# Kernel tuning notes

Measured on AMD Instinct MI355X. Metric: run time of the kernel, lower is better.

The kernel has to match this reference:

```python
import jax, jax.numpy as jnp
import numpy as np

N = 10000      # nodes
E = 320000     # edges (avg degree 32)
G = 32         # graphs in batch
L = 6          # layers
C0, C1, C2 = 128, 64, 32   # irreps channels: 128x0e + 64x1e + 32x2e
H = 4          # attention heads
NB = 128       # radial basis
RAD = 64       # radial MLP width (fc_neurons=[64,64])
F = 512        # irreps_feature = 512x0e
T = 1          # num_targets
MAXR = 5.0


def setup_inputs() -> dict:
    key = jax.random.key(0)
    ks = iter(jax.random.split(key, 64))
    def nrm(shape, scale):
        return jax.random.normal(next(ks), shape, jnp.float32) * scale
    inp = {}
    inp['pos'] = jax.random.normal(next(ks), (N, 3), jnp.float32) * 3.0
    inp['node_atom'] = jax.random.randint(next(ks), (N,), 0, 5)
    inp['batch'] = jnp.sort(jax.random.randint(next(ks), (N,), 0, G))
    inp['edge_src'] = jax.random.randint(next(ks), (E,), 0, N)
    inp['edge_dst'] = jax.random.randint(next(ks), (E,), 0, N)
    inp['atom_emb'] = nrm((5, C0), 1.0)
    inp['Wrad1'] = nrm((L, NB, RAD), NB ** -0.5)
    inp['brad1'] = jnp.zeros((L, RAD), jnp.float32)
    inp['Wrad2'] = nrm((L, RAD, RAD), RAD ** -0.5)
    inp['brad2'] = jnp.zeros((L, RAD), jnp.float32)
    inp['Ws_src'] = nrm((L, C0, C0), C0 ** -0.5)
    inp['Ww_s'] = nrm((L, RAD, C0), RAD ** -0.5)
    inp['Ws_v'] = nrm((L, C0, C1), C0 ** -0.5)
    inp['Ww_v'] = nrm((L, RAD, C1), RAD ** -0.5)
    inp['Wv_v'] = nrm((L, C1, C1), C1 ** -0.5)
    inp['Ww_vv'] = nrm((L, RAD, C1), RAD ** -0.5)
    inp['Ws_t'] = nrm((L, C0, C2), C0 ** -0.5)
    inp['Ww_t'] = nrm((L, RAD, C2), RAD ** -0.5)
    inp['Wt_t'] = nrm((L, C2, C2), C2 ** -0.5)
    inp['Ww_tt'] = nrm((L, RAD, C2), RAD ** -0.5)
    inp['attn_a'] = nrm((L, H, C0 // H), (C0 // H) ** -0.5)
    inp['Wo_s'] = nrm((L, C0, C0), C0 ** -0.5)
    inp['Wo_v'] = nrm((L, C1, C1), C1 ** -0.5)
    inp['Wo_t'] = nrm((L, C2, C2), C2 ** -0.5)
    inp['g_s'] = jnp.ones((L, C0), jnp.float32)
    inp['b_s'] = jnp.zeros((L, C0), jnp.float32)
    inp['g_v'] = jnp.ones((L, C1), jnp.float32)
    inp['g_t'] = jnp.ones((L, C2), jnp.float32)
    inp['W_feat'] = nrm((C0, F), C0 ** -0.5)
    inp['b_feat'] = jnp.zeros((F,), jnp.float32)
    inp['W_out1'] = nrm((F, 1), F ** -0.5)
    inp['b_out1'] = jnp.zeros((1,), jnp.float32)
    inp['W_read'] = nrm((1, T), 1.0)
    inp['b_read'] = jnp.zeros((T,), jnp.float32)
    return inp


def reference(pos, node_atom, batch, edge_src, edge_dst, atom_emb,
              Wrad1, brad1, Wrad2, brad2, Ws_src, Ww_s, Ws_v, Ww_v,
              Wv_v, Ww_vv, Ws_t, Ww_t, Wt_t, Ww_tt, attn_a,
              Wo_s, Wo_v, Wo_t, g_s, b_s, g_v, g_t,
              W_feat, b_feat, W_out1, b_out1, W_read, b_read):
    eps = 1e-6
    # node features per irrep: scalars s [N,C0], vectors v [N,C1,3], l=2 t [N,C2,5]
    s = atom_emb[node_atom]
    v = jnp.zeros((N, C1, 3), s.dtype)
    t = jnp.zeros((N, C2, 5), s.dtype)
    # edge geometry (shared across layers)
    rel = pos[edge_dst] - pos[edge_src]            # [E,3]
    d = jnp.sqrt(jnp.sum(rel * rel, -1) + eps)     # [E]
    u = rel / d[:, None]
    centers = jnp.linspace(0.0, MAXR, NB)
    width = MAXR / NB
    rbf = jnp.exp(-0.5 * ((d[:, None] - centers[None, :]) / width) ** 2)  # [E,NB]
    x_, y_, z_ = u[:, 0], u[:, 1], u[:, 2]
    s3, s5, s15 = jnp.sqrt(3.0), jnp.sqrt(5.0), jnp.sqrt(15.0)
    sh1 = s3 * u                                   # [E,3]  l=1 spherical harmonics
    sh2 = jnp.stack([s15 * x_ * y_, s15 * y_ * z_, 0.5 * s5 * (3 * z_ * z_ - 1.0),
                     s15 * x_ * z_, 0.5 * s15 * (x_ * x_ - y_ * y_)], -1)  # [E,5]
    for l in range(L):
        # radial MLP on RBF -> per-edge tensor-product weights
        w = jax.nn.silu(jax.nn.silu(rbf @ Wrad1[l] + brad1[l]) @ Wrad2[l] + brad2[l])  # [E,RAD]
        s_e = s[edge_src]
        # tensor-product messages: 0e x Yl paths + self (l x 0e) paths
        msg_s = (s_e @ Ws_src[l]) * (w @ Ww_s[l])                                        # [E,C0]
        msg_v = ((s_e @ Ws_v[l]) * (w @ Ww_v[l]))[:, :, None] * sh1[:, None, :] \
              + jnp.einsum('eci,cd->edi', v[edge_src], Wv_v[l]) * (w @ Ww_vv[l])[:, :, None]  # [E,C1,3]
        msg_t = ((s_e @ Ws_t[l]) * (w @ Ww_t[l]))[:, :, None] * sh2[:, None, :] \
              + jnp.einsum('ecm,cd->edm', t[edge_src], Wt_t[l]) * (w @ Ww_tt[l])[:, :, None]  # [E,C2,5]
        # multi-head attention over incoming edges (softmax per dst node)
        msg_sh = msg_s.reshape(E, H, C0 // H)
        logit = jnp.einsum('ehc,hc->eh', msg_sh, attn_a[l])                              # [E,H]
        mx = jax.ops.segment_max(logit, edge_dst, num_segments=N)
        ex = jnp.exp(logit - mx[edge_dst])
        den = jax.ops.segment_sum(ex, edge_dst, num_segments=N) + 1e-9
        alpha = ex / den[edge_dst]                                                       # [E,H]
        agg_s = jax.ops.segment_sum(alpha[:, :, None] * msg_sh, edge_dst, num_segments=N).reshape(N, C0)
        agg_v = jax.ops.segment_sum(alpha[:, :, None, None] * msg_v.reshape(E, H, C1 // H, 3),
                                    edge_dst, num_segments=N).reshape(N, C1, 3)
        agg_t = jax.ops.segment_sum(alpha[:, :, None, None] * msg_t.reshape(E, H, C2 // H, 5),
                                    edge_dst, num_segments=N).reshape(N, C2, 5)
        # output projection + residual
        s = s + agg_s @ Wo_s[l]
        v = v + jnp.einsum('nci,cd->ndi', agg_v, Wo_v[l])
        t = t + jnp.einsum('ncm,cd->ndm', agg_t, Wo_t[l])
        # equivariant layer norm
        mu = jnp.mean(s, -1, keepdims=True)
        var = jnp.mean((s - mu) ** 2, -1, keepdims=True)
        s = (s - mu) / jnp.sqrt(var + eps) * g_s[l] + b_s[l]
        v = v / jnp.sqrt(jnp.mean(jnp.sum(v * v, -1), -1) + eps)[:, None, None] * g_v[l][None, :, None]
        t = t / jnp.sqrt(jnp.mean(jnp.sum(t * t, -1), -1) + eps)[:, None, None] * g_t[l][None, :, None]
    # 512x0e feature head -> per-node scalar -> sum pool per graph -> readout Linear(1,T)
    feat = jax.nn.gelu(s @ W_feat + b_feat)
    node_e = feat @ W_out1 + b_out1                      # [N,1]
    graph = jax.ops.segment_sum(node_e, batch, num_segments=G)  # [G,1]
    return graph @ W_read + b_read                       # [G,T]
```

## Files before the change

### kernel.cpp

```cpp
#include <hip/hip_runtime.h>
#include <math.h>

#define NN 10000
#define EE 320000
#define GG 32
#define LL 6
#define TABN 2048
#define TABB (TABN / 64)
#define DTAB 5.45f
#define DCUT 5.4f

__device__ __forceinline__ float fsilu(float x) { return x / (1.0f + __expf(-x)); }
__device__ __forceinline__ float fgelu(float x) {
  float y = 0.7978845608f * (x + 0.044715f * x * x * x);
  float t = 1.0f - 2.0f / (__expf(2.0f * y) + 1.0f);
  return 0.5f * x * (1.0f + t);
}

__global__ void k_hist(const int* __restrict__ dst, int* __restrict__ deg) {
  int e = blockIdx.x * blockDim.x + threadIdx.x;
  if (e < EE) atomicAdd(&deg[dst[e]], 1);
}

__global__ void k_scan(const int* __restrict__ cnt, int* __restrict__ off, int n) {
// ... 450 lines not shown
    float nm2 = fmaxf(rm2, l2), nm3 = fmaxf(rm3, l3);
    float f0 = __expf(rm0 - nm0), f1 = __expf(rm1 - nm1);
    float f2 = __expf(rm2 - nm2), f3 = __expf(rm3 - nm3);
    float w0 = __expf(l0 - nm0), w1 = __expf(l1 - nm1);
    float w2 = __expf(l2 - nm2), w3 = __expf(l3 - nm3);
    rm0 = nm0; rm1 = nm1; rm2 = nm2; rm3 = nm3;
    rs0 = rs0 * f0 + w0; rs1 = rs1 * f1 + w1;
    rs2 = rs2 * f2 + w2; rs3 = rs3 * f3 + w3;
    float fS0 = (lane < 32) ? f0 : f1;
    float fS1 = (lane < 32) ? f2 : f3;
    float wS0 = (lane < 32) ? w0 : w1;
    float wS1 = (lane < 32) ? w2 : w3;
    as0 = as0 * fS0 + wS0 * m0;
    as1 = as1 * fS1 + wS1 * m1;
    const float* gv0 = gvL + (size_t)i0 * 128;
    float2 p0 = *(const float2*)&gv0[2 * lane];
    float2 p1 = *(const float2*)&gv0[128 + 2 * lane];
    float gav = p0.x * g1 + p1.x * f;
    float gbv = p0.y * g1 + p1.y * f;
    float fV = (lane < 16) ? f0 : (lane < 32) ? f1 : (lane < 48) ? f2 : f3;
    float wV = (lane < 16) ? w0 : (lane < 32) ? w1 : (lane < 48) ? w2 : w3;
    float avv = sWv[(size_t)sn * 64 + lane] * gav;
    float4 s1 = *(const float4*)&sh_a[(size_t)a * 8];
    float4 s2 = *(const float4*)&sh_a[(size_t)a * 8 + 4];
    const float* vp = &vW[(size_t)sn * 192 + lane];
    av0 = av0 * fV + wV * (avv * s1.x + vp[0] * gbv);
    av1 = av1 * fV + wV * (avv * s1.y + vp[64] * gbv);
    av2 = av2 * fV + wV * (avv * s1.z + vp[128] * gbv);
    if (lane < 32) {
      const float* gt0 = gtL + (size_t)i0 * 64;
      float2 q0 = *(const float2*)&gt0[2 * lt];
      float2 q1 = *(const float2*)&gt0[64 + 2 * lt];
      float gat = q0.x * g1 + q1.x * f;
      float gbt = q0.y * g1 + q1.y * f;
      float fT = (lane < 8) ? f0 : (lane < 16) ? f1 : (lane < 24) ? f2 : f3;
      float wT = (lane < 8) ? w0 : (lane < 16) ? w1 : (lane < 24) ? w2 : w3;
      float att = sWt[(size_t)sn * 32 + lane] * gat;
      const float* tp = &tW[(size_t)sn * 160 + lane];
      at0 = at0 * fT + wT * (att * s1.w + tp[0] * gbt);
      at1 = at1 * fT + wT * (att * s2.x + tp[32] * gbt);
      at2 = at2 * fT + wT * (att * s2.y + tp[64] * gbt);
      at3 = at3 * fT + wT * (att * s2.z + tp[96] * gbt);
      at4 = at4 * fT + wT * (att * s2.w + tp[128] * gbt);
    }
  }
  if (ninact > 0) {
    rs0 += (float)ninact * __expf(-rm0);
    rs1 += (float)ninact * __expf(-rm1);
    rs2 += (float)ninact * __expf(-rm2);
    rs3 += (float)ninact * __expf(-rm3);
  }
  float r0 = 1.0f / (rs0 + 1e-9f), r1 = 1.0f / (rs1 + 1e-9f);
  float r2 = 1.0f / (rs2 + 1e-9f), r3 = 1.0f / (rs3 + 1e-9f);
  float rS0 = (lane < 32) ? r0 : r1;
  float rS1 = (lane < 32) ? r2 : r3;
  float rV = (lane < 16) ? r0 : (lane < 32) ? r1 : (lane < 48) ? r2 : r3;
  agg_s[(size_t)n * 128 + lane] = as0 * rS0;
  agg_s[(size_t)n * 128 + 64 + lane] = as1 * rS1;
  agg_v[(size_t)n * 192 + lane * 3 + 0] = av0 * rV;
  agg_v[(size_t)n * 192 + lane * 3 + 1] = av1 * rV;
  agg_v[(size_t)n * 192 + lane * 3 + 2] = av2 * rV;
  if (lane < 32) {
    float rT = (lane < 8) ? r0 : (lane < 16) ? r1 : (lane < 24) ? r2 : r3;
    agg_t[(size_t)n * 160 + lane * 5 + 0] = at0 * rT;
    agg_t[(size_t)n * 160 + lane * 5 + 1] = at1 * rT;
    agg_t[(size_t)n * 160 + lane * 5 + 2] = at2 * rT;
    agg_t[(size_t)n * 160 + lane * 5 + 3] = at3 * rT;
    agg_t[(size_t)n * 160 + lane * 5 + 4] = at4 * rT;
  }
}

__global__ __launch_bounds__(256) void k_node_fused(
    float* __restrict__ s, float* __restrict__ v, float* __restrict__ t,
    const float* __restrict__ agg_s, const float* __restrict__ agg_v,
    const float* __restrict__ agg_t, const float* __restrict__ Wo_s,
    const float* __restrict__ Wo_v, const float* __restrict__ Wo_t,
    const float* __restrict__ g_s, const float* __restrict__ b_s,
    const float* __restrict__ g_v, const float* __restrict__ g_t,
    const float* __restrict__ Ws_src, const float* __restrict__ Ws_v,
    const float* __restrict__ Ws_t, const float* __restrict__ Wv_v,
    const float* __restrict__ Wt_t, float* __restrict__ sWsrc,
    float* __restrict__ sWv, float* __restrict__ sWt, float* __restrict__ vW,
    float* __restrict__ tW) {
  int nb = blockIdx.x * 8;
  int tid = threadIdx.x;
  __shared__ float bin[8][193];
  __shared__ float sN[8][129];
  __shared__ float vN[8][193];
  __shared__ float tN[8][161];
  for (int idx = tid; idx < 8 * 128; idx += 256) {
    int n = idx >> 7, c = idx & 127;
    bin[n][c] = agg_s[(size_t)(nb + n) * 128 + c];
  }
  __syncthreads();
  {
    int col = tid & 127, ng = tid >> 7;
    float acc[4];
    #pragma unroll
    for (int n = 0; n < 4; n++) acc[n] = s[(size_t)(nb + ng * 4 + n) * 128 + col];
    for (int c = 0; c < 128; c++) {
      float w = Wo_s[c * 128 + col];
      #pragma unroll
      for (int n = 0; n < 4; n++) acc[n] += bin[ng * 4 + n][c] * w;
    }
    #pragma unroll
    for (int n = 0; n < 4; n++) sN[ng * 4 + n][col] = acc[n];
  }
  __syncthreads();
  for (int idx = tid; idx < 8 * 192; idx += 256) {
    int n = idx / 192, c = idx % 192;
    bin[n][c] = agg_v[(size_t)(nb + n) * 192 + c];
  }
  {
    int node = tid >> 5, q = tid & 31;
    float sm = 0.f, sq = 0.f;
    #pragma unroll
    for (int u = 0; u < 4; u++) {
      float x = sN[node][q * 4 + u];
      sm += x; sq += x * x;
    }
    sm += __shfl_xor(sm, 1); sq += __shfl_xor(sq, 1);
    sm += __shfl_xor(sm, 2); sq += __shfl_xor(sq, 2);
    sm += __shfl_xor(sm, 4); sq += __shfl_xor(sq, 4);
    sm += __shfl_xor(sm, 8); sq += __shfl_xor(sq, 8);
    sm += __shfl_xor(sm, 16); sq += __shfl_xor(sq, 16);
    float mu = sm / 128.0f;
    float var = sq / 128.0f - mu * mu;
    if (var < 0.f) var = 0.f;
    float ri = rsqrtf(var + 1e-6f);
    #pragma unroll
    for (int u = 0; u < 4; u++) {
      int c = q * 4 + u;
      float y = (sN[node][c] - mu) * ri * g_s[c] + b_s[c];
      sN[node][c] = y;
      s[(size_t)(nb + node) * 128 + c] = y;
    }
  }
  __syncthreads();
  {
    int dd = tid & 63, ng = tid >> 6;
    float acc[2][3];
    #pragma unroll
    for (int n = 0; n < 2; n++)
      #pragma unroll
      for (int i = 0; i < 3; i++)
        acc[n][i] = v[(size_t)(nb + ng * 2 + n) * 192 + dd * 3 + i];
    for (int c = 0; c < 64; c++) {
      float w = Wo_v[c * 64 + dd];
      #pragma unroll
      for (int n = 0; n < 2; n++) {
        acc[n][0] += bin[ng * 2 + n][c * 3 + 0] * w;
        acc[n][1] += bin[ng * 2 + n][c * 3 + 1] * w;
        acc[n][2] += bin[ng * 2 + n][c * 3 + 2] * w;
      }
    }
    #pragma unroll
    for (int n = 0; n < 2; n++)
      #pragma unroll
      for (int i = 0; i < 3; i++) vN[ng * 2 + n][dd * 3 + i] = acc[n][i];
  }
  __syncthreads();
  for (int idx = tid; idx < 8 * 160; idx += 256) {
    int n = idx / 160, c = idx % 160;
    bin[n][c] = agg_t[(size_t)(nb + n) * 160 + c];
  }
  {
    int node = tid >> 5, q = tid & 31;
    float ssq = 0.f;
    #pragma unroll
    for (int u = 0; u < 6; u++) {
      float x = vN[node][q * 6 + u];
      ssq += x * x;
    }
    ssq += __shfl_xor(ssq, 1);
    ssq += __shfl_xor(ssq, 2);
    ssq += __shfl_xor(ssq, 4);
    ssq += __shfl_xor(ssq, 8);
    ssq += __shfl_xor(ssq, 16);
    float ri = rsqrtf(ssq / 64.0f + 1e-6f);
    #pragma unroll
    for (int u = 0; u < 6; u++) {
      int o = q * 6 + u;
      float y = vN[node][o] * ri * g_v[o / 3];
      vN[node][o] = y;
      v[(size_t)(nb + node) * 192 + o] = y;
    }
  }
  __syncthreads();
  {
    int dd = tid & 31, ng = tid >> 5;
    float acc[5];
    #pragma unroll
    for (int m = 0; m < 5; m++)
      acc[m] = t[(size_t)(nb + ng) * 160 + dd * 5 + m];
    for (int c = 0; c < 32; c++) {
      float w = Wo_t[c * 32 + dd];
      #pragma unroll
      for (int m = 0; m < 5; m++) acc[m] += bin[ng][c * 5 + m] * w;
    }
    #pragma unroll
    for (int m = 0; m < 5; m++) tN[ng][dd * 5 + m] = acc[m];
  }
  __syncthreads();
  {
    int node = tid >> 5, q = tid & 31;
    float ssq = 0.f;
    #pragma unroll
    for (int u = 0; u < 5; u++) {
      float x = tN[node][q * 5 + u];
      ssq += x * x;
    }
    ssq += __shfl_xor(ssq, 1);
    ssq += __shfl_xor(ssq, 2);
    ssq += __shfl_xor(ssq, 4);
    ssq += __shfl_xor(ssq, 8);
    ssq += __shfl_xor(ssq, 16);
    float ri = rsqrtf(ssq / 32.0f + 1e-6f);
    float gq = g_t[q];
    #pragma unroll
    for (int u = 0; u < 5; u++) {
      int o = q * 5 + u;
      float y = tN[node][o] * ri * gq;
      tN[node][o] = y;
      t[(size_t)(nb + node) * 160 + o] = y;
    }
  }
  __syncthreads();
  {
    int col = tid & 127, ng = tid >> 7;
    float acc[4] = {0, 0, 0, 0};
    for (int c = 0; c < 128; c++) {
      float w = Ws_src[c * 128 + col];
      #pragma unroll
      for (int n = 0; n < 4; n++) acc[n] += sN[ng * 4 + n][c] * w;
    }
    #pragma unroll
    for (int n = 0; n < 4; n++) sWsrc[(size_t)(nb + ng * 4 + n) * 128 + col] = acc[n];
  }
  {
    int col = tid & 63, ng = tid >> 6;
    float acc[2] = {0, 0};
    for (int c = 0; c < 128; c++) {
      float w = Ws_v[c * 64 + col];
      acc[0] += sN[ng * 2 + 0][c] * w;
      acc[1] += sN[ng * 2 + 1][c] * w;
    }
    sWv[(size_t)(nb + ng * 2 + 0) * 64 + col] = acc[0];
    sWv[(size_t)(nb + ng * 2 + 1) * 64 + col] = acc[1];
  }
  {
    int col = tid & 31, ng = tid >> 5;
    float acc = 0.f;
    for (int c = 0; c < 128; c++) acc += sN[ng][c] * Ws_t[c * 32 + col];
    sWt[(size_t)(nb + ng) * 32 + col] = acc;
  }
  {
    int dd = tid & 63, ng = tid >> 6;
    float acc[2][3] = {};
    for (int c = 0; c < 64; c++) {
      float w = Wv_v[c * 64 + dd];
      #pragma unroll
      for (int n = 0; n < 2; n++) {
        acc[n][0] += vN[ng * 2 + n][c * 3 + 0] * w;
        acc[n][1] += vN[ng * 2 + n][c * 3 + 1] * w;
        acc[n][2] += vN[ng * 2 + n][c * 3 + 2] * w;
      }
    }
    #pragma unroll
    for (int n = 0; n < 2; n++) {
      size_t b = (size_t)(nb + ng * 2 + n) * 192 + dd;
      vW[b + 0] = acc[n][0];
      vW[b + 64] = acc[n][1];
      vW[b + 128] = acc[n][2];
    }
  }
  {
    int dd = tid & 31, ng = tid >> 5;
    float acc[5] = {};
    for (int c = 0; c < 32; c++) {
      float w = Wt_t[c * 32 + dd];
      #pragma unroll
      for (int m = 0; m < 5; m++) acc[m] += tN[ng][c * 5 + m] * w;
    }
    size_t b = (size_t)(nb + ng) * 160 + dd;
    #pragma unroll
    for (int m = 0; m < 5; m++) tW[b + m * 32] = acc[m];
  }
}

__global__ __launch_bounds__(256) void k_node_up(
    float* __restrict__ s, float* __restrict__ v, float* __restrict__ t,
    const float* __restrict__ agg_s, const float* __restrict__ agg_v,
    const float* __restrict__ agg_t, const float* __restrict__ Wo_s,
    const float* __restrict__ Wo_v, const float* __restrict__ Wo_t,
    const float* __restrict__ g_s, const float* __restrict__ b_s,
    const float* __restrict__ g_v, const float* __restrict__ g_t) {
  int nb = blockIdx.x * 8;
  int tid = threadIdx.x;
  __shared__ float bin[8][193];
  __shared__ float sN[8][129];
  __shared__ float vN[8][193];
  __shared__ float tN[8][161];
  for (int idx = tid; idx < 8 * 128; idx += 256) {
    int n = idx >> 7, c = idx & 127;
    bin[n][c] = agg_s[(size_t)(nb + n) * 128 + c];
  }
  __syncthreads();
  {
    int col = tid & 127, ng = tid >> 7;
    float acc[4];
    #pragma unroll
    for (int n = 0; n < 4; n++) acc[n] = s[(size_t)(nb + ng * 4 + n) * 128 + col];
    for (int c = 0; c < 128; c++) {
      float w = Wo_s[c * 128 + col];
      #pragma unroll
      for (int n = 0; n < 4; n++) acc[n] += bin[ng * 4 + n][c] * w;
    }
    #pragma unroll
    for (int n = 0; n < 4; n++) sN[ng * 4 + n][col] = acc[n];
  }
  __syncthreads();
  for (int idx = tid; idx < 8 * 192; idx += 256) {
    int n = idx / 192, c = idx % 192;
    bin[n][c] = agg_v[(size_t)(nb + n) * 192 + c];
  }
  {
    int node = tid >> 5, q = tid & 31;
    float sm = 0.f, sq = 0.f;
    #pragma unroll
    for (int u = 0; u < 4; u++) {
      float x = sN[node][q * 4 + u];
      sm += x; sq += x * x;
    }
    sm += __shfl_xor(sm, 1); sq += __shfl_xor(sq, 1);
    sm += __shfl_xor(sm, 2); sq += __shfl_xor(sq, 2);
    sm += __shfl_xor(sm, 4); sq += __shfl_xor(sq, 4);
    sm += __shfl_xor(sm, 8); sq += __shfl_xor(sq, 8);
    sm += __shfl_xor(sm, 16); sq += __shfl_xor(sq, 16);
    float mu = sm / 128.0f;
    float var = sq / 128.0f - mu * mu;
    if (var < 0.f) var = 0.f;
    float ri = rsqrtf(var + 1e-6f);
    #pragma unroll
    for (int u = 0; u < 4; u++) {
      int c = q * 4 + u;
      s[(size_t)(nb + node) * 128 + c] = (sN[node][c] - mu) * ri * g_s[c] + b_s[c];
    }
  }
  __syncthreads();
  {
    int dd = tid & 63, ng = tid >> 6;
    float acc[2][3];
    #pragma unroll
    for (int n = 0; n < 2; n++)
      #pragma unroll
      for (int i = 0; i < 3; i++)
        acc[n][i] = v[(size_t)(nb + ng * 2 + n) * 192 + dd * 3 + i];
    for (int c = 0; c < 64; c++) {
      float w = Wo_v[c * 64 + dd];
      #pragma unroll
      for (int n = 0; n < 2; n++) {
        acc[n][0] += bin[ng * 2 + n][c * 3 + 0] * w;
        acc[n][1] += bin[ng * 2 + n][c * 3 + 1] * w;
        acc[n][2] += bin[ng * 2 + n][c * 3 + 2] * w;
      }
    }
    #pragma unroll
    for (int n = 0; n < 2; n++)
      #pragma unroll
      for (int i = 0; i < 3; i++) vN[ng * 2 + n][dd * 3 + i] = acc[n][i];
  }
  __syncthreads();
  for (int idx = tid; idx < 8 * 160; idx += 256) {
    int n = idx / 160, c = idx % 160;
    bin[n][c] = agg_t[(size_t)(nb + n) * 160 + c];
  }
  {
    int node = tid >> 5, q = tid & 31;
    float ssq = 0.f;
    #pragma unroll
    for (int u = 0; u < 6; u++) {
      float x = vN[node][q * 6 + u];
      ssq += x * x;
    }
    ssq += __shfl_xor(ssq, 1);
    ssq += __shfl_xor(ssq, 2);
    ssq += __shfl_xor(ssq, 4);
    ssq += __shfl_xor(ssq, 8);
    ssq += __shfl_xor(ssq, 16);
    float ri = rsqrtf(ssq / 64.0f + 1e-6f);
    #pragma unroll
    for (int u = 0; u < 6; u++) {
      int o = q * 6 + u;
      v[(size_t)(nb + node) * 192 + o] = vN[node][o] * ri * g_v[o / 3];
    }
  }
  __syncthreads();
  {
    int dd = tid & 31, ng = tid >> 5;
    float acc[5];
    #pragma unroll
    for (int m = 0; m < 5; m++)
      acc[m] = t[(size_t)(nb + ng) * 160 + dd * 5 + m];
    for (int c = 0; c < 32; c++) {
      float w = Wo_t[c * 32 + dd];
      #pragma unroll
      for (int m = 0; m < 5; m++) acc[m] += bin[ng][c * 5 + m] * w;
    }
    #pragma unroll
    for (int m = 0; m < 5; m++) tN[ng][dd * 5 + m] = acc[m];
  }
  __syncthreads();
  {
    int node = tid >> 5, q = tid & 31;
    float ssq = 0.f;
    #pragma unroll
    for (int u = 0; u < 5; u++) {
      float x = tN[node][q * 5 + u];
      ssq += x * x;
    }
    ssq += __shfl_xor(ssq, 1);
    ssq += __shfl_xor(ssq, 2);
    ssq += __shfl_xor(ssq, 4);
    ssq += __shfl_xor(ssq, 8);
    ssq += __shfl_xor(ssq, 16);
    float ri = rsqrtf(ssq / 32.0f + 1e-6f);
    float gq = g_t[q];
    #pragma unroll
    for (int u = 0; u < 5; u++) {
      int o = q * 5 + u;
      t[(size_t)(nb + node) * 160 + o] = tN[node][o] * ri * gq;
    }
  }
}

__global__ __launch_bounds__(256) void k_readout(
    const float* __restrict__ s, const int* __restrict__ batch,
    const float* __restrict__ W_feat, const float* __restrict__ b_feat,
    const float* __restrict__ W_out1, const float* __restrict__ b_out1,
    float* __restrict__ graph) {
  __shared__ float st[64][129];
  __shared__ float gacc[GG];
  int nb = blockIdx.x * 64;
  int fb = blockIdx.y;
  for (int idx = threadIdx.x; idx < 64 * 128; idx += 256) {
    int nl = idx >> 7, c = idx & 127;
    int n = nb + nl;
    st[nl][c] = (n < NN) ? s[(size_t)n * 128 + c] : 0.f;
  }
  if (threadIdx.x < GG) gacc[threadIdx.x] = 0.f;
  __syncthreads();
  int wv = threadIdx.x >> 6, lane = threadIdx.x & 63;
  int fg = lane & 15;
  int ns = lane >> 4;
  int f0 = fb * 64 + fg * 4;
  int nodeb = wv * 16 + ns * 4;
  float acc[4][4];
  #pragma unroll
  for (int nn = 0; nn < 4; nn++)
    #pragma unroll
    for (int k = 0; k < 4; k++) acc[nn][k] = b_feat[f0 + k];
  #pragma unroll 4
  for (int c = 0; c < 128; c++) {
    float4 wq = *(const float4*)&W_feat[(size_t)c * 512 + f0];
    #pragma unroll
    for (int nn = 0; nn < 4; nn++) {
      float sv = st[nodeb + nn][c];
      acc[nn][0] += sv * wq.x;
      acc[nn][1] += sv * wq.y;
      acc[nn][2] += sv * wq.z;
      acc[nn][3] += sv * wq.w;
    }
  }
  float wo[4];
  #pragma unroll
  for (int k = 0; k < 4; k++) wo[k] = W_out1[f0 + k];
  float ep[4];
  #pragma unroll
  for (int nn = 0; nn < 4; nn++) {
    float p = 0.f;
    #pragma unroll
    for (int k = 0; k < 4; k++) p += fgelu(acc[nn][k]) * wo[k];
    ep[nn] = p;
  }
  #pragma unroll
  for (int mm = 1; mm < 16; mm <<= 1) {
    #pragma unroll
    for (int nn = 0; nn < 4; nn++) ep[nn] += __shfl_xor(ep[nn], mm);
  }
  if (fg == 0) {
    #pragma unroll
    for (int nn = 0; nn < 4; nn++) {
      int n = nb + nodeb + nn;
      if (n < NN) {
        float e = ep[nn];
        if (fb == 0) e += b_out1[0];
        atomicAdd(&gacc[batch[n]], e);
      }
    }
  }
  __syncthreads();
  if (threadIdx.x < GG && gacc[threadIdx.x] != 0.f)
    atomicAdd(&graph[threadIdx.x], gacc[threadIdx.x]);
}

__global__ void k_finalize(const float* __restrict__ graph, const float* __restrict__ W_read,
                           const float* __restrict__ b_read, float* __restrict__ out) {
  int g = threadIdx.x;
  if (g < GG) out[g] = graph[g] * W_read[0] + b_read[0];
}

extern "C" void kernel_launch(void* const* d_in, const int* in_sizes, int n_in,
                              void* d_out, int out_size, void* d_ws, size_t ws_size,
                              hipStream_t stream) {
  const float* pos = (const float*)d_in[0];
// ... 30 lines not shown
  const float* b_out1 = (const float*)d_in[31];
  const float* W_read = (const float*)d_in[32];
  const float* b_read = (const float*)d_in[33];
  float* out = (float*)d_out;

  char* base = (char*)d_ws;
  size_t off = 0;
  auto alloc = [&](size_t bytes) -> char* {
    off = (off + 255) & ~(size_t)255;
    char* p = base + off;
    off += bytes;
    return p;
  };
  int* deg = (int*)alloc(NN * 4);
  int* row_off = (int*)alloc((NN + 1) * 4);
  int* cursor = (int*)alloc(NN * 4);
  int* perm = (int*)alloc((size_t)EE * 4);
  float* d_csr = (float*)alloc((size_t)EE * 4);
  int* acnt = (int*)alloc(NN * 4);
  int* act_off = (int*)alloc((NN + 1) * 4);
  int* act_idx = (int*)alloc((size_t)EE * 4);
  int* dbkt = (int*)alloc(128 * 4);
  int* dboff = (int*)alloc(129 * 4);
  int* dbcur = (int*)alloc(128 * 4);
  int* order = (int*)alloc(NN * 4);
  float* d_a = (float*)alloc((size_t)EE * 4);
  int* src_a = (int*)alloc((size_t)EE * 4);
  float* sh_a = (float*)alloc((size_t)EE * 8 * 4);
  float* wtab = (float*)alloc((size_t)LL * TABN * 64 * 4);
  float* gs_tab = (float*)alloc((size_t)LL * TABN * 128 * 4);
  float* gv_tab = (float*)alloc((size_t)LL * TABN * 128 * 4);
  float* gt_tab = (float*)alloc((size_t)LL * TABN * 64 * 4);
  float* s = (float*)alloc((size_t)NN * 128 * 4);
  float* v = (float*)alloc((size_t)NN * 192 * 4);
  float* t = (float*)alloc((size_t)NN * 160 * 4);
  float* sWsrc = (float*)alloc((size_t)NN * 128 * 4);
  float* sWv = (float*)alloc((size_t)NN * 64 * 4);
  float* sWt = (float*)alloc((size_t)NN * 32 * 4);
  float* vW = (float*)alloc((size_t)NN * 192 * 4);
  float* tW = (float*)alloc((size_t)NN * 160 * 4);
  float* agg_s = (float*)alloc((size_t)NN * 128 * 4);
  float* agg_v = (float*)alloc((size_t)NN * 192 * 4);
  float* agg_t = (float*)alloc((size_t)NN * 160 * 4);
  float* graph = (float*)alloc(GG * 4);

  hipMemsetAsync(deg, 0, NN * 4, stream);
  hipMemsetAsync(cursor, 0, NN * 4, stream);
  hipMemsetAsync(dbkt, 0, 128 * 4, stream);
  hipMemsetAsync(dbcur, 0, 128 * 4, stream);
  hipMemsetAsync(graph, 0, GG * 4, stream);
  hipMemsetAsync(v, 0, (size_t)NN * 192 * 4, stream);
  hipMemsetAsync(t, 0, (size_t)NN * 160 * 4, stream);
  hipMemsetAsync(vW, 0, (size_t)NN * 192 * 4, stream);
  hipMemsetAsync(tW, 0, (size_t)NN * 160 * 4, stream);

  k_hist<<<(EE + 255) / 256, 256, 0, stream>>>(edst, deg);
  k_scan<<<1, 1024, 0, stream>>>(deg, row_off, NN);
  k_scatter<<<(EE + 255) / 256, 256, 0, stream>>>(edst, row_off, cursor, perm);
  k_geom_d<<<(EE + 255) / 256, 256, 0, stream>>>(pos, esrc, edst, perm, d_csr);
  k_act_cnt<<<(NN + 255) / 256, 256, 0, stream>>>(row_off, d_csr, acnt);
  k_scan<<<1, 1024, 0, stream>>>(acnt, act_off, NN);
  k_act_fill<<<(NN + 255) / 256, 256, 0, stream>>>(row_off, d_csr, act_off, act_idx);
  k_dhist<<<(NN + 255) / 256, 256, 0, stream>>>(acnt, dbkt);
  k_scan<<<1, 1024, 0, stream>>>(dbkt, dboff, 128);
  k_dscatter<<<(NN + 255) / 256, 256, 0, stream>>>(acnt, dboff, dbcur, order);
  k_geom_act<<<(EE + 255) / 256, 256, 0, stream>>>(act_idx, perm, esrc, edst, pos, act_off,
                                                   d_a, src_a, sh_a);
  k_build_wtab<<<LL * TABB, 256, 0, stream>>>(Wrad1, brad1, Wrad2, brad2, wtab);
  k_build_gs<<<LL * TABB, 256, 0, stream>>>(wtab, Ww_s, gs_tab);
  k_build_gv<<<LL * TABB, 256, 0, stream>>>(wtab, Ww_v, Ww_vv, gv_tab);
  k_build_gt<<<LL * TABB, 256, 0, stream>>>(wtab, Ww_t, Ww_tt, gt_tab);
  k_init_s<<<(NN * 128 + 255) / 256, 256, 0, stream>>>(node_atom, atom_emb, s);

  k_node_tf0<<<NN / 16, 256, 0, stream>>>(s, Ws_src, Ws_v, Ws_t, sWsrc, sWv, sWt);

  for (int l = 0; l < LL; l++) {
    const float* gsL = gs_tab + (size_t)l * TABN * 128;
    const float* gvL = gv_tab + (size_t)l * TABN * 128;
    const float* gtL = gt_tab + (size_t)l * TABN * 64;
    k_mega<<<NN / 4, 256, 0, stream>>>(row_off, act_off, order, src_a, d_a, gsL, gvL, gtL,
                                       attn_a + (size_t)l * 128,
                                       sWsrc, sWv, sWt, vW, tW, sh_a, agg_s, agg_v, agg_t);
    if (l < LL - 1) {
      k_node_fused<<<NN / 8, 256, 0, stream>>>(
          s, v, t, agg_s, agg_v, agg_t,
          Wo_s + (size_t)l * 128 * 128, Wo_v + (size_t)l * 64 * 64,
          Wo_t + (size_t)l * 32 * 32,
          g_s + (size_t)l * 128, b_s + (size_t)l * 128,
          g_v + (size_t)l * 64, g_t + (size_t)l * 32,
          Ws_src + (size_t)(l + 1) * 128 * 128, Ws_v + (size_t)(l + 1) * 128 * 64,
          Ws_t + (size_t)(l + 1) * 128 * 32, Wv_v + (size_t)(l + 1) * 64 * 64,
          Wt_t + (size_t)(l + 1) * 32 * 32,
          sWsrc, sWv, sWt, vW, tW);
    } else {
      k_node_up<<<NN / 8, 256, 0, stream>>>(s, v, t, agg_s, agg_v, agg_t,
                                            Wo_s + (size_t)l * 128 * 128,
                                            Wo_v + (size_t)l * 64 * 64, Wo_t + (size_t)l * 32 * 32,
                                            g_s + (size_t)l * 128, b_s + (size_t)l * 128,
                                            g_v + (size_t)l * 64, g_t + (size_t)l * 32);
    }
  }
  dim3 rg((NN + 63) / 64, 8);
  k_readout<<<rg, 256, 0, stream>>>(s, batch, W_feat, b_feat, W_out1, b_out1, graph);
  k_finalize<<<1, 64, 0, stream>>>(graph, W_read, b_read, out);
}
```

Measured before the change: 1.135 ms.

## Restructure node update kernels to one wavefront per node without block barriers

The node-update kernels now map one 64-lane wavefront to each node (4 nodes per 256-thread block) instead of sharing 8 nodes across the whole block. All __syncthreads barriers are replaced by per-wave LDS staging with s_waitcnt, and layer-norm reductions are done fully with wave shuffles. This removes block-wide synchronisation and lets waves progress independently. In exchange, each weight element is reused across fewer nodes (1 per wave rather than 2-4), so weight traffic from cache rises, and the kernel relies on in-order LDS behaviour within a wave for correctness.

New measurement: 1.226 ms. 8.0% more time.

```diff
diff --git a/kernel.cpp b/kernel.cpp
--- a/kernel.cpp
+++ b/kernel.cpp
@@ -556,209 +556,156 @@
     const float* __restrict__ Wt_t, float* __restrict__ sWsrc,
     float* __restrict__ sWv, float* __restrict__ sWt, float* __restrict__ vW,
     float* __restrict__ tW) {
-  int nb = blockIdx.x * 8;
-  int tid = threadIdx.x;
-  __shared__ float bin[8][193];
-  __shared__ float sN[8][129];
-  __shared__ float vN[8][193];
-  __shared__ float tN[8][161];
-  for (int idx = tid; idx < 8 * 128; idx += 256) {
-    int n = idx >> 7, c = idx & 127;
-    bin[n][c] = agg_s[(size_t)(nb + n) * 128 + c];
-  }
-  __syncthreads();
-  {
-    int col = tid & 127, ng = tid >> 7;
-    float acc[4];
-    #pragma unroll
-    for (int n = 0; n < 4; n++) acc[n] = s[(size_t)(nb + ng * 4 + n) * 128 + col];
-    for (int c = 0; c < 128; c++) {
-      float w = Wo_s[c * 128 + col];
-      #pragma unroll
-      for (int n = 0; n < 4; n++) acc[n] += bin[ng * 4 + n][c] * w;
-    }
-    #pragma unroll
-    for (int n = 0; n < 4; n++) sN[ng * 4 + n][col] = acc[n];
-  }
-  __syncthreads();
-  for (int idx = tid; idx < 8 * 192; idx += 256) {
-    int n = idx / 192, c = idx % 192;
-    bin[n][c] = agg_v[(size_t)(nb + n) * 192 + c];
-  }
-  {
-    int node = tid >> 5, q = tid & 31;
-    float sm = 0.f, sq = 0.f;
-    #pragma unroll
-    for (int u = 0; u < 4; u++) {
-      float x = sN[node][q * 4 + u];
-      sm += x; sq += x * x;
-    }
-    sm += __shfl_xor(sm, 1); sq += __shfl_xor(sq, 1);
-    sm += __shfl_xor(sm, 2); sq += __shfl_xor(sq, 2);
-    sm += __shfl_xor(sm, 4); sq += __shfl_xor(sq, 4);
-    sm += __shfl_xor(sm, 8); sq += __shfl_xor(sq, 8);
-    sm += __shfl_xor(sm, 16); sq += __shfl_xor(sq, 16);
-    float mu = sm / 128.0f;
-    float var = sq / 128.0f - mu * mu;
-    if (var < 0.f) var = 0.f;
-    float ri = rsqrtf(var + 1e-6f);
-    #pragma unroll
-    for (int u = 0; u < 4; u++) {
-      int c = q * 4 + u;
-      float y = (sN[node][c] - mu) * ri * g_s[c] + b_s[c];
-      sN[node][c] = y;
-      s[(size_t)(nb + node) * 128 + c] = y;
-    }
-  }
-  __syncthreads();
-  {
-    int dd = tid & 63, ng = tid >> 6;
-    float acc[2][3];
-    #pragma unroll
-    for (int n = 0; n < 2; n++)
-      #pragma unroll
-      for (int i = 0; i < 3; i++)
-        acc[n][i] = v[(size_t)(nb + ng * 2 + n) * 192 + dd * 3 + i];
-    for (int c = 0; c < 64; c++) {
-      float w = Wo_v[c * 64 + dd];
-      #pragma unroll
-      for (int n = 0; n < 2; n++) {
-        acc[n][0] += bin[ng * 2 + n][c * 3 + 0] * w;
-        acc[n][1] += bin[ng * 2 + n][c * 3 + 1] * w;
-        acc[n][2] += bin[ng * 2 + n][c * 3 + 2] * w;
-      }
-    }
-    #pragma unroll
-    for (int n = 0; n < 2; n++)
-      #pragma unroll
-      for (int i = 0; i < 3; i++) vN[ng * 2 + n][dd * 3 + i] = acc[n][i];
-  }
-  __syncthreads();
-  for (int idx = tid; idx < 8 * 160; idx += 256) {
-    int n = idx / 160, c = idx % 160;
-    bin[n][c] = agg_t[(size_t)(nb + n) * 160 + c];
-  }
-  {
-    int node = tid >> 5, q = tid & 31;
-    float ssq = 0.f;
-    #pragma unroll
-    for (int u = 0; u < 6; u++) {
-      float x = vN[node][q * 6 + u];
-      ssq += x * x;
-    }
-    ssq += __shfl_xor(ssq, 1);
-    ssq += __shfl_xor(ssq, 2);
-    ssq += __shfl_xor(ssq, 4);
-    ssq += __shfl_xor(ssq, 8);
-    ssq += __shfl_xor(ssq, 16);
-    float ri = rsqrtf(ssq / 64.0f + 1e-6f);
-    #pragma unroll
-    for (int u = 0; u < 6; u++) {
-      int o = q * 6 + u;
-      float y = vN[node][o] * ri * g_v[o / 3];
-      vN[node][o] = y;
-      v[(size_t)(nb + node) * 192 + o] = y;
-    }
-  }
-  __syncthreads();
-  {
-    int dd = tid & 31, ng = tid >> 5;
-    float acc[5];
-    #pragma unroll
-    for (int m = 0; m < 5; m++)
-      acc[m] = t[(size_t)(nb + ng) * 160 + dd * 5 + m];
-    for (int c = 0; c < 32; c++) {
-      float w = Wo_t[c * 32 + dd];
-      #pragma unroll
-      for (int m = 0; m < 5; m++) acc[m] += bin[ng][c * 5 + m] * w;
-    }
-    #pragma unroll
-    for (int m = 0; m < 5; m++) tN[ng][dd * 5 + m] = acc[m];
-  }
-  __syncthreads();
-  {
-    int node = tid >> 5, q = tid & 31;
-    float ssq = 0.f;
-    #pragma unroll
-    for (int u = 0; u < 5; u++) {
-      float x = tN[node][q * 5 + u];
-      ssq += x * x;
-    }
-    ssq += __shfl_xor(ssq, 1);
-    ssq += __shfl_xor(ssq, 2);
-    ssq += __shfl_xor(ssq, 4);
-    ssq += __shfl_xor(ssq, 8);
-    ssq += __shfl_xor(ssq, 16);
-    float ri = rsqrtf(ssq / 32.0f + 1e-6f);
-    float gq = g_t[q];
-    #pragma unroll
-    for (int u = 0; u < 5; u++) {
-      int o = q * 5 + u;
-      float y = tN[node][o] * ri * gq;
-      tN[node][o] = y;
-      t[(size_t)(nb + node) * 160 + o] = y;
-    }
-  }
-  __syncthreads();
-  {
-    int col = tid & 127, ng = tid >> 7;
-    float acc[4] = {0, 0, 0, 0};
-    for (int c = 0; c < 128; c++) {
-      float w = Ws_src[c * 128 + col];
-      #pragma unroll
-      for (int n = 0; n < 4; n++) acc[n] += sN[ng * 4 + n][c] * w;
-    }
-    #pragma unroll
-    for (int n = 0; n < 4; n++) sWsrc[(size_t)(nb + ng * 4 + n) * 128 + col] = acc[n];
-  }
-  {
-    int col = tid & 63, ng = tid >> 6;
-    float acc[2] = {0, 0};
-    for (int c = 0; c < 128; c++) {
-      float w = Ws_v[c * 64 + col];
-      acc[0] += sN[ng * 2 + 0][c] * w;
-      acc[1] += sN[ng * 2 + 1][c] * w;
-    }
-    sWv[(size_t)(nb + ng * 2 + 0) * 64 + col] = acc[0];
-    sWv[(size_t)(nb + ng * 2 + 1) * 64 + col] = acc[1];
-  }
-  {
-    int col = tid & 31, ng = tid >> 5;
-    float acc = 0.f;
-    for (int c = 0; c < 128; c++) acc += sN[ng][c] * Ws_t[c * 32 + col];
-    sWt[(size_t)(nb + ng) * 32 + col] = acc;
-  }
-  {
-    int dd = tid & 63, ng = tid >> 6;
-    float acc[2][3] = {};
-    for (int c = 0; c < 64; c++) {
-      float w = Wv_v[c * 64 + dd];
-      #pragma unroll
-      for (int n = 0; n < 2; n++) {
-        acc[n][0] += vN[ng * 2 + n][c * 3 + 0] * w;
-        acc[n][1] += vN[ng * 2 + n][c * 3 + 1] * w;
-        acc[n][2] += vN[ng * 2 + n][c * 3 + 2] * w;
-      }
-    }
-    #pragma unroll
-    for (int n = 0; n < 2; n++) {
-      size_t b = (size_t)(nb + ng * 2 + n) * 192 + dd;
-      vW[b + 0] = acc[n][0];
-      vW[b + 64] = acc[n][1];
-      vW[b + 128] = acc[n][2];
-    }
-  }
-  {
-    int dd = tid & 31, ng = tid >> 5;
-    float acc[5] = {};
-    for (int c = 0; c < 32; c++) {
-      float w = Wt_t[c * 32 + dd];
-      #pragma unroll
-      for (int m = 0; m < 5; m++) acc[m] += tN[ng][c * 5 + m] * w;
-    }
-    size_t b = (size_t)(nb + ng) * 160 + dd;
-    #pragma unroll
-    for (int m = 0; m < 5; m++) tW[b + m * 32] = acc[m];
+  int wv = threadIdx.x >> 6, lane = threadIdx.x & 63;
+  int lt = lane & 31;
+  int n = blockIdx.x * 4 + wv;
+  __shared__ float sN[4][128];
+  __shared__ float vN[4][192];
+  __shared__ float tN[4][160];
+  __shared__ float stg[4][192];
+  float a0 = agg_s[(size_t)n * 128 + lane];
+  float a1 = agg_s[(size_t)n * 128 + 64 + lane];
+  float acc0 = s[(size_t)n * 128 + lane];
+  float acc1 = s[(size_t)n * 128 + 64 + lane];
+  stg[wv][lane] = a0;
+  stg[wv][64 + lane] = a1;
+  asm volatile("s_waitcnt lgkmcnt(0)" ::: "memory");
+  #pragma unroll 8
+  for (int c = 0; c < 128; c++) {
+    float a = stg[wv][c];
+    acc0 += a * Wo_s[c * 128 + lane];
+    acc1 += a * Wo_s[c * 128 + 64 + lane];
+  }
+  float bv0 = agg_v[(size_t)n * 192 + lane];
+  float bv1 = agg_v[(size_t)n * 192 + 64 + lane];
+  float bv2 = agg_v[(size_t)n * 192 + 128 + lane];
+  float vo0 = v[(size_t)n * 192 + lane * 3 + 0];
+  float vo1 = v[(size_t)n * 192 + lane * 3 + 1];
+  float vo2 = v[(size_t)n * 192 + lane * 3 + 2];
+  float sm = acc0 + acc1, sq = acc0 * acc0 + acc1 * acc1;
+  #pragma unroll
+  for (int m = 1; m < 64; m <<= 1) { sm += __shfl_xor(sm, m); sq += __shfl_xor(sq, m); }
+  float mu = sm / 128.0f;
+  float var = sq / 128.0f - mu * mu;
+  if (var < 0.f) var = 0.f;
+  float ri = rsqrtf(var + 1e-6f);
+  float y0 = (acc0 - mu) * ri * g_s[lane] + b_s[lane];
+  float y1 = (acc1 - mu) * ri * g_s[64 + lane] + b_s[64 + lane];
+  s[(size_t)n * 128 + lane] = y0;
+  s[(size_t)n * 128 + 64 + lane] = y1;
+  sN[wv][lane] = y0;
+  sN[wv][64 + lane] = y1;
+  stg[wv][lane] = bv0;
+  stg[wv][64 + lane] = bv1;
+  stg[wv][128 + lane] = bv2;
+  asm volatile("s_waitcnt lgkmcnt(0)" ::: "memory");
+  float av0 = vo0, av1 = vo1, av2 = vo2;
+  #pragma unroll 8
+  for (int c = 0; c < 64; c++) {
+    float w = Wo_v[c * 64 + lane];
+    av0 += stg[wv][c * 3 + 0] * w;
+    av1 += stg[wv][c * 3 + 1] * w;
+    av2 += stg[wv][c * 3 + 2] * w;
+  }
+  float bt0 = agg_t[(size_t)n * 160 + lane];
+  float bt1 = agg_t[(size_t)n * 160 + 64 + lane];
+  float bt2 = (lane < 32) ? agg_t[(size_t)n * 160 + 128 + lane] : 0.f;
+  float to0 = t[(size_t)n * 160 + lt * 5 + 0];
+  float to1 = t[(size_t)n * 160 + lt * 5 + 1];
+  float to2 = t[(size_t)n * 160 + lt * 5 + 2];
+  float to3 = t[(size_t)n * 160 + lt * 5 + 3];
+  float to4 = t[(size_t)n * 160 + lt * 5 + 4];
+  float ssq = av0 * av0 + av1 * av1 + av2 * av2;
+  #pragma unroll
+  for (int m = 1; m < 64; m <<= 1) ssq += __shfl_xor(ssq, m);
+  float riv = rsqrtf(ssq / 64.0f + 1e-6f);
+  float gv = g_v[lane];
+  float vy0 = av0 * riv * gv, vy1 = av1 * riv * gv, vy2 = av2 * riv * gv;
+  v[(size_t)n * 192 + lane * 3 + 0] = vy0;
+  v[(size_t)n * 192 + lane * 3 + 1] = vy1;
+  v[(size_t)n * 192 + lane * 3 + 2] = vy2;
+  vN[wv][lane * 3 + 0] = vy0;
+  vN[wv][lane * 3 + 1] = vy1;
+  vN[wv][lane * 3 + 2] = vy2;
+  stg[wv][lane] = bt0;
+  stg[wv][64 + lane] = bt1;
+  if (lane < 32) stg[wv][128 + lane] = bt2;
+  asm volatile("s_waitcnt lgkmcnt(0)" ::: "memory");
+  float at0 = to0, at1 = to1, at2 = to2, at3 = to3, at4 = to4;
+  #pragma unroll 4
+  for (int c = 0; c < 32; c++) {
+    float w = Wo_t[c * 32 + lt];
+    at0 += stg[wv][c * 5 + 0] * w;
+    at1 += stg[wv][c * 5 + 1] * w;
+    at2 += stg[wv][c * 5 + 2] * w;
+    at3 += stg[wv][c * 5 + 3] * w;
+    at4 += stg[wv][c * 5 + 4] * w;
+  }
+  float ssqt = at0 * at0 + at1 * at1 + at2 * at2 + at3 * at3 + at4 * at4;
+  #pragma unroll
+  for (int m = 1; m < 32; m <<= 1) ssqt += __shfl_xor(ssqt, m);
+  float rit = rsqrtf(ssqt / 32.0f + 1e-6f);
+  float gt = g_t[lt];
+  float ty0 = at0 * rit * gt, ty1 = at1 * rit * gt, ty2 = at2 * rit * gt;
+  float ty3 = at3 * rit * gt, ty4 = at4 * rit * gt;
+  if (lane < 32) {
+    t[(size_t)n * 160 + lt * 5 + 0] = ty0;
+    t[(size_t)n * 160 + lt * 5 + 1] = ty1;
+    t[(size_t)n * 160 + lt * 5 + 2] = ty2;
+    t[(size_t)n * 160 + lt * 5 + 3] = ty3;
+    t[(size_t)n * 160 + lt * 5 + 4] = ty4;
+    tN[wv][lt * 5 + 0] = ty0;
+    tN[wv][lt * 5 + 1] = ty1;
+    tN[wv][lt * 5 + 2] = ty2;
+    tN[wv][lt * 5 + 3] = ty3;
+    tN[wv][lt * 5 + 4] = ty4;
+  }
+  asm volatile("s_waitcnt lgkmcnt(0)" ::: "memory");
+  float c0 = 0.f, c1 = 0.f;
+  #pragma unroll 8
+  for (int c = 0; c < 128; c++) {
+    float a = sN[wv][c];
+    c0 += a * Ws_src[c * 128 + lane];
+    c1 += a * Ws_src[c * 128 + 64 + lane];
+  }
+  sWsrc[(size_t)n * 128 + lane] = c0;
+  sWsrc[(size_t)n * 128 + 64 + lane] = c1;
+  float cv = 0.f, ct = 0.f;
+  #pragma unroll 8
+  for (int c = 0; c < 128; c++) {
+    float a = sN[wv][c];
+    cv += a * Ws_v[c * 64 + lane];
+    ct += a * Ws_t[c * 32 + lt];
+  }
+  sWv[(size_t)n * 64 + lane] = cv;
+  if (lane < 32) sWt[(size_t)n * 32 + lane] = ct;
+  float w0 = 0.f, w1 = 0.f, w2 = 0.f;
+  #pragma unroll 8
+  for (int c = 0; c < 64; c++) {
+    float w = Wv_v[c * 64 + lane];
+    w0 += vN[wv][c * 3 + 0] * w;
+    w1 += vN[wv][c * 3 + 1] * w;
+    w2 += vN[wv][c * 3 + 2] * w;
+  }
+  vW[(size_t)n * 192 + lane] = w0;
+  vW[(size_t)n * 192 + 64 + lane] = w1;
+  vW[(size_t)n * 192 + 128 + lane] = w2;
+  float u0 = 0.f, u1 = 0.f, u2 = 0.f, u3 = 0.f, u4 = 0.f;
+  #pragma unroll 4
+  for (int c = 0; c < 32; c++) {
+    float w = Wt_t[c * 32 + lt];
+    u0 += tN[wv][c * 5 + 0] * w;
+    u1 += tN[wv][c * 5 + 1] * w;
+    u2 += tN[wv][c * 5 + 2] * w;
+    u3 += tN[wv][c * 5 + 3] * w;
+    u4 += tN[wv][c * 5 + 4] * w;
+  }
+  if (lane < 32) {
+    tW[(size_t)n * 160 + lt] = u0;
+    tW[(size_t)n * 160 + 32 + lt] = u1;
+    tW[(size_t)n * 160 + 64 + lt] = u2;
+    tW[(size_t)n * 160 + 96 + lt] = u3;
+    tW[(size_t)n * 160 + 128 + lt] = u4;
   }
 }
 
@@ -769,142 +716,91 @@
     const float* __restrict__ Wo_v, const float* __restrict__ Wo_t,
     const float* __restrict__ g_s, const float* __restrict__ b_s,
     const float* __restrict__ g_v, const float* __restrict__ g_t) {
-  int nb = blockIdx.x * 8;
-  int tid = threadIdx.x;
-  __shared__ float bin[8][193];
-  __shared__ float sN[8][129];
-  __shared__ float vN[8][193];
-  __shared__ float tN[8][161];
-  for (int idx = tid; idx < 8 * 128; idx += 256) {
-    int n = idx >> 7, c = idx & 127;
-    bin[n][c] = agg_s[(size_t)(nb + n) * 128 + c];
-  }
-  __syncthreads();
-  {
-    int col = tid & 127, ng = tid >> 7;
-    float acc[4];
-    #pragma unroll
-    for (int n = 0; n < 4; n++) acc[n] = s[(size_t)(nb + ng * 4 + n) * 128 + col];
-    for (int c = 0; c < 128; c++) {
-      float w = Wo_s[c * 128 + col];
-      #pragma unroll
-      for (int n = 0; n < 4; n++) acc[n] += bin[ng * 4 + n][c] * w;
-    }
-    #pragma unroll
-    for (int n = 0; n < 4; n++) sN[ng * 4 + n][col] = acc[n];
-  }
-  __syncthreads();
-  for (int idx = tid; idx < 8 * 192; idx += 256) {
-    int n = idx / 192, c = idx % 192;
-    bin[n][c] = agg_v[(size_t)(nb + n) * 192 + c];
-  }
-  {
-    int node = tid >> 5, q = tid & 31;
-    float sm = 0.f, sq = 0.f;
-    #pragma unroll
-    for (int u = 0; u < 4; u++) {
-      float x = sN[node][q * 4 + u];
-      sm += x; sq += x * x;
-    }
-    sm += __shfl_xor(sm, 1); sq += __shfl_xor(sq, 1);
-    sm += __shfl_xor(sm, 2); sq += __shfl_xor(sq, 2);
-    sm += __shfl_xor(sm, 4); sq += __shfl_xor(sq, 4);
-    sm += __shfl_xor(sm, 8); sq += __shfl_xor(sq, 8);
-    sm += __shfl_xor(sm, 16); sq += __shfl_xor(sq, 16);
-    float mu = sm / 128.0f;
-    float var = sq / 128.0f - mu * mu;
-    if (var < 0.f) var = 0.f;
-    float ri = rsqrtf(var + 1e-6f);
-    #pragma unroll
-    for (int u = 0; u < 4; u++) {
-      int c = q * 4 + u;
-      s[(size_t)(nb + node) * 128 + c] = (sN[node][c] - mu) * ri * g_s[c] + b_s[c];
-    }
-  }
-  __syncthreads();
-  {
-    int dd = tid & 63, ng = tid >> 6;
-    float acc[2][3];
-    #pragma unroll
-    for (int n = 0; n < 2; n++)
-      #pragma unroll
-      for (int i = 0; i < 3; i++)
-        acc[n][i] = v[(size_t)(nb + ng * 2 + n) * 192 + dd * 3 + i];
-    for (int c = 0; c < 64; c++) {
-      float w = Wo_v[c * 64 + dd];
-      #pragma unroll
-      for (int n = 0; n < 2; n++) {
-        acc[n][0] += bin[ng * 2 + n][c * 3 + 0] * w;
-        acc[n][1] += bin[ng * 2 + n][c * 3 + 1] * w;
-        acc[n][2] += bin[ng * 2 + n][c * 3 + 2] * w;
-      }
-    }
-    #pragma unroll
-    for (int n = 0; n < 2; n++)
-      #pragma unroll
-      for (int i = 0; i < 3; i++) vN[ng * 2 + n][dd * 3 + i] = acc[n][i];
-  }
-  __syncthreads();
-  for (int idx = tid; idx < 8 * 160; idx += 256) {
-    int n = idx / 160, c = idx % 160;
-    bin[n][c] = agg_t[(size_t)(nb + n) * 160 + c];
-  }
-  {
-    int node = tid >> 5, q = tid & 31;
-    float ssq = 0.f;
-    #pragma unroll
-    for (int u = 0; u < 6; u++) {
-      float x = vN[node][q * 6 + u];
-      ssq += x * x;
-    }
-    ssq += __shfl_xor(ssq, 1);
-    ssq += __shfl_xor(ssq, 2);
-    ssq += __shfl_xor(ssq, 4);
-    ssq += __shfl_xor(ssq, 8);
-    ssq += __shfl_xor(ssq, 16);
-    float ri = rsqrtf(ssq / 64.0f + 1e-6f);
-    #pragma unroll
-    for (int u = 0; u < 6; u++) {
-      int o = q * 6 + u;
-      v[(size_t)(nb + node) * 192 + o] = vN[node][o] * ri * g_v[o / 3];
-    }
-  }
-  __syncthreads();
-  {
-    int dd = tid & 31, ng = tid >> 5;
-    float acc[5];
-    #pragma unroll
-    for (int m = 0; m < 5; m++)
-      acc[m] = t[(size_t)(nb + ng) * 160 + dd * 5 + m];
-    for (int c = 0; c < 32; c++) {
-      float w = Wo_t[c * 32 + dd];
-      #pragma unroll
-      for (int m = 0; m < 5; m++) acc[m] += bin[ng][c * 5 + m] * w;
-    }
-    #pragma unroll
-    for (int m = 0; m < 5; m++) tN[ng][dd * 5 + m] = acc[m];
-  }
-  __syncthreads();
-  {
-    int node = tid >> 5, q = tid & 31;
-    float ssq = 0.f;
-    #pragma unroll
-    for (int u = 0; u < 5; u++) {
-      float x = tN[node][q * 5 + u];
-      ssq += x * x;
-    }
-    ssq += __shfl_xor(ssq, 1);
-    ssq += __shfl_xor(ssq, 2);
-    ssq += __shfl_xor(ssq, 4);
-    ssq += __shfl_xor(ssq, 8);
-    ssq += __shfl_xor(ssq, 16);
-    float ri = rsqrtf(ssq / 32.0f + 1e-6f);
-    float gq = g_t[q];
-    #pragma unroll
-    for (int u = 0; u < 5; u++) {
-      int o = q * 5 + u;
-      t[(size_t)(nb + node) * 160 + o] = tN[node][o] * ri * gq;
-    }
+  int wv = threadIdx.x >> 6, lane = threadIdx.x & 63;
+  int lt = lane & 31;
+  int n = blockIdx.x * 4 + wv;
+  __shared__ float stg[4][192];
+  float a0 = agg_s[(size_t)n * 128 + lane];
+  float a1 = agg_s[(size_t)n * 128 + 64 + lane];
+  float acc0 = s[(size_t)n * 128 + lane];
+  float acc1 = s[(size_t)n * 128 + 64 + lane];
+  stg[wv][lane] = a0;
+  stg[wv][64 + lane] = a1;
+  asm volatile("s_waitcnt lgkmcnt(0)" ::: "memory");
+  #pragma unroll 8
+  for (int c = 0; c < 128; c++) {
+    float a = stg[wv][c];
+    acc0 += a * Wo_s[c * 128 + lane];
+    acc1 += a * Wo_s[c * 128 + 64 + lane];
+  }
+  float bv0 = agg_v[(size_t)n * 192 + lane];
+  float bv1 = agg_v[(size_t)n * 192 + 64 + lane];
+  float bv2 = agg_v[(size_t)n * 192 + 128 + lane];
+  float vo0 = v[(size_t)n * 192 + lane * 3 + 0];
+  float vo1 = v[(size_t)n * 192 + lane * 3 + 1];
+  float vo2 = v[(size_t)n * 192 + lane * 3 + 2];
+  float sm = acc0 + acc1, sq = acc0 * acc0 + acc1 * acc1;
+  #pragma unroll
+  for (int m = 1; m < 64; m <<= 1) { sm += __shfl_xor(sm, m); sq += __shfl_xor(sq, m); }
+  float mu = sm / 128.0f;
+  float var = sq / 128.0f - mu * mu;
+  if (var < 0.f) var = 0.f;
+  float ri = rsqrtf(var + 1e-6f);
+  s[(size_t)n * 128 + lane] = (acc0 - mu) * ri * g_s[lane] + b_s[lane];
+  s[(size_t)n * 128 + 64 + lane] = (acc1 - mu) * ri * g_s[64 + lane] + b_s[64 + lane];
+  stg[wv][lane] = bv0;
+  stg[wv][64 + lane] = bv1;
+  stg[wv][128 + lane] = bv2;
+  asm volatile("s_waitcnt lgkmcnt(0)" ::: "memory");
+  float av0 = vo0, av1 = vo1, av2 = vo2;
+  #pragma unroll 8
+  for (int c = 0; c < 64; c++) {
+    float w = Wo_v[c * 64 + lane];
+    av0 += stg[wv][c * 3 + 0] * w;
+    av1 += stg[wv][c * 3 + 1] * w;
+    av2 += stg[wv][c * 3 + 2] * w;
+  }
+  float bt0 = agg_t[(size_t)n * 160 + lane];
+  float bt1 = agg_t[(size_t)n * 160 + 64 + lane];
+  float bt2 = (lane < 32) ? agg_t[(size_t)n * 160 + 128 + lane] : 0.f;
+  float to0 = t[(size_t)n * 160 + lt * 5 + 0];
+  float to1 = t[(size_t)n * 160 + lt * 5 + 1];
+  float to2 = t[(size_t)n * 160 + lt * 5 + 2];
+  float to3 = t[(size_t)n * 160 + lt * 5 + 3];
+  float to4 = t[(size_t)n * 160 + lt * 5 + 4];
+  float ssq = av0 * av0 + av1 * av1 + av2 * av2;
+  #pragma unroll
+  for (int m = 1; m < 64; m <<= 1) ssq += __shfl_xor(ssq, m);
+  float riv = rsqrtf(ssq / 64.0f + 1e-6f);
+  float gv = g_v[lane];
+  v[(size_t)n * 192 + lane * 3 + 0] = av0 * riv * gv;
+  v[(size_t)n * 192 + lane * 3 + 1] = av1 * riv * gv;
+  v[(size_t)n * 192 + lane * 3 + 2] = av2 * riv * gv;
+  stg[wv][lane] = bt0;
+  stg[wv][64 + lane] = bt1;
+  if (lane < 32) stg[wv][128 + lane] = bt2;
+  asm volatile("s_waitcnt lgkmcnt(0)" ::: "memory");
+  float at0 = to0, at1 = to1, at2 = to2, at3 = to3, at4 = to4;
+  #pragma unroll 4
+  for (int c = 0; c < 32; c++) {
+    float w = Wo_t[c * 32 + lt];
+    at0 += stg[wv][c * 5 + 0] * w;
+    at1 += stg[wv][c * 5 + 1] * w;
+    at2 += stg[wv][c * 5 + 2] * w;
+    at3 += stg[wv][c * 5 + 3] * w;
+    at4 += stg[wv][c * 5 + 4] * w;
+  }
+  float ssqt = at0 * at0 + at1 * at1 + at2 * at2 + at3 * at3 + at4 * at4;
+  #pragma unroll
+  for (int m = 1; m < 32; m <<= 1) ssqt += __shfl_xor(ssqt, m);
+  float rit = rsqrtf(ssqt / 32.0f + 1e-6f);
+  float gt = g_t[lt];
+  if (lane < 32) {
+    t[(size_t)n * 160 + lt * 5 + 0] = at0 * rit * gt;
+    t[(size_t)n * 160 + lt * 5 + 1] = at1 * rit * gt;
+    t[(size_t)n * 160 + lt * 5 + 2] = at2 * rit * gt;
+    t[(size_t)n * 160 + lt * 5 + 3] = at3 * rit * gt;
+    t[(size_t)n * 160 + lt * 5 + 4] = at4 * rit * gt;
   }
 }
 
@@ -1101,7 +997,7 @@
                                        attn_a + (size_t)l * 128,
                                        sWsrc, sWv, sWt, vW, tW, sh_a, agg_s, agg_v, agg_t);
     if (l < LL - 1) {
-      k_node_fused<<<NN / 8, 256, 0, stream>>>(
+      k_node_fused<<<NN / 4, 256, 0, stream>>>(
           s, v, t, agg_s, agg_v, agg_t,
           Wo_s + (size_t)l * 128 * 128, Wo_v + (size_t)l * 64 * 64,
           Wo_t + (size_t)l * 32 * 32,
@@ -1112,7 +1008,7 @@
           Wt_t + (size_t)(l + 1) * 32 * 32,
           sWsrc, sWv, sWt, vW, tW);
     } else {
-      k_node_up<<<NN / 8, 256, 0, stream>>>(s, v, t, agg_s, agg_v, agg_t,
+      k_node_up<<<NN / 4, 256, 0, stream>>>(s, v, t, agg_s, agg_v, agg_t,
                                             Wo_s + (size_t)l * 128 * 128,
                                             Wo_v + (size_t)l * 64 * 64, Wo_t + (size_t)l * 32 * 32,
                                             g_s + (size_t)l * 128, b_s + (size_t)l * 128,
```
